# Performance work log

Measured on AMD Instinct MI355X. Metric: run time of the kernel, lower is better.

The kernel has to match this reference:

```python
import jax, jax.numpy as jnp
import numpy as np


def setup_inputs() -> dict:
    key = jax.random.key(0)
    kx, kq, kb, kc = jax.random.split(key, 4)
    N, D = 16384, 1024
    x = jax.random.normal(kx, (N, D), dtype=jnp.float32)
    Q = jax.random.normal(kq, (D, D), dtype=jnp.float32)
    b = jax.random.normal(kb, (D,), dtype=jnp.float32)
    c = jax.random.normal(kc, (1,), dtype=jnp.float32)
    return {"x": x, "Q": Q, "b": b, "c": c}


def reference(x, Q, b, c):
    # y_i = x_i^T Q x_i + b^T x_i + c  (same math as diag(x @ Q @ x.T)
    # without materializing the NxN matrix)
    xQ = x @ Q                                # [N, D]
    quad = jnp.sum(xQ * x, axis=-1)           # [N]
    y = quad + x @ b + c                       # [N] (c broadcasts from [1])
    return y[:, None]                          # [N, 1]
```

## Files before the change

### kernel.cpp

```cpp
#include <hip/hip_runtime.h>
#include <hip/hip_bf16.h>


#define DD 1024
#define KSTEPS 32
#define NTILE 32
#define LDS_ROW 520

typedef short v8s __attribute__((ext_vector_type(8)));
typedef float v4f __attribute__((ext_vector_type(4)));

__device__ __forceinline__ short f2b(float f) {
    union { __hip_bfloat16 h; short s; } u;
    u.h = __float2bfloat16(f);
    return u.s;
}

__global__ __launch_bounds__(512, 2)
void quad_kernel(const float* __restrict__ x, const float* __restrict__ Q,
                 const float* __restrict__ bvec, const float* __restrict__ cptr,
                 float* __restrict__ y)
{
    __shared__ short lq[2][16 * LDS_ROW];

    const int tid  = threadIdx.x;
    const int lane = tid & 63;
    const int wave = tid >> 6;
    const int quad = lane >> 4;
    const int l15  = lane & 15;

    const int half = blockIdx.x >> 7;
    const int rblk = blockIdx.x & 127;
    const int row_base = rblk * 128 + wave * 16;
    const int t0 = half * NTILE;

    const float cc = (half == 0) ? cptr[0] : 0.f;

    v8s afrag[KSTEPS];
    {
        const float* xr = x + (size_t)(row_base + l15) * DD + quad * 8;
        #pragma unroll
        for (int kt = 0; kt < KSTEPS; ++kt) {
            const float4 f0 = *(const float4*)(xr + kt * 32);
            const float4 f1 = *(const float4*)(xr + kt * 32 + 4);
            v8s a;
            a[0]=f2b(f0.x); a[1]=f2b(f0.y); a[2]=f2b(f0.z); a[3]=f2b(f0.w);
            a[4]=f2b(f1.x); a[5]=f2b(f1.y); a[6]=f2b(f1.z); a[7]=f2b(f1.w);
            afrag[kt] = a;
            asm volatile("" : "+a"(afrag[kt]));
        }
    }

    int s_nn[4], s_k4[4];
    #pragma unroll
    for (int i = 0; i < 4; ++i) {
        const int idx = tid + i * 512;
        s_nn[i] = idx >> 7;
        s_k4[i] = idx & 127;
    }

    float4 pf[4];
    #pragma unroll
    for (int i = 0; i < 4; ++i)
        pf[i] = *(const float4*)(Q + (size_t)(t0 * 16 + s_nn[i]) * DD + s_k4[i] * 4);

    float acc[4] = {0.f, 0.f, 0.f, 0.f};
    v4f cf = {0.f, 0.f, 0.f, 0.f};
    float xv[4], bn;

    const short* bp0 = &lq[0][l15 * LDS_ROW + quad * 8];
    const short* bp1 = &lq[1][l15 * LDS_ROW + quad * 8];

    for (int t = 0; t < NTILE; ++t) {
        const int tg = t0 + t;

        #pragma unroll
        for (int i = 0; i < 4; ++i) {
            const float4 f = pf[i];
            short4 s;
            s.x=f2b(f.x); s.y=f2b(f.y); s.z=f2b(f.z); s.w=f2b(f.w);
            *(short4*)&lq[0][s_nn[i] * LDS_ROW + s_k4[i] * 4] = s;
        }
        #pragma unroll
        for (int i = 0; i < 4; ++i)
            pf[i] = *(const float4*)(Q + (size_t)(tg * 16 + s_nn[i]) * DD + 512 + s_k4[i] * 4);
        {
            const int n = tg * 16 + l15;
            bn = bvec[n];
            const float* xc = x + (size_t)(row_base + quad * 4) * DD + n;
            #pragma unroll
            for (int r = 0; r < 4; ++r) xv[r] = xc[(size_t)r * DD];
        }
        __syncthreads();
        #pragma unroll
        for (int s = 0; s < 16; ++s) {
            const v8s bfrag = *(const v8s*)(bp0 + s * 32);
            cf = __builtin_amdgcn_mfma_f32_16x16x32_bf16(afrag[s], bfrag, cf, 0, 0, 0);
        }

        #pragma unroll
        for (int i = 0; i < 4; ++i) {
            const float4 f = pf[i];
            short4 s;
            s.x=f2b(f.x); s.y=f2b(f.y); s.z=f2b(f.z); s.w=f2b(f.w);
            *(short4*)&lq[1][s_nn[i] * LDS_ROW + s_k4[i] * 4] = s;
        }
        if (t + 1 < NTILE) {
            #pragma unroll
            for (int i = 0; i < 4; ++i)
                pf[i] = *(const float4*)(Q + (size_t)((tg + 1) * 16 + s_nn[i]) * DD + s_k4[i] * 4);
        }
        __syncthreads();
        #pragma unroll
        for (int s = 0; s < 16; ++s) {
            const v8s bfrag = *(const v8s*)(bp1 + s * 32);
            cf = __builtin_amdgcn_mfma_f32_16x16x32_bf16(afrag[16 + s], bfrag, cf, 0, 0, 0);
        }

        #pragma unroll
        for (int r = 0; r < 4; ++r) acc[r] += (cf[r] + bn) * xv[r];
        cf = (v4f){0.f, 0.f, 0.f, 0.f};
    }

    #pragma unroll
    for (int r = 0; r < 4; ++r) {
        float v = acc[r];
        v += __shfl_xor(v, 1);
        v += __shfl_xor(v, 2);
        v += __shfl_xor(v, 4);
        v += __shfl_xor(v, 8);
        if (l15 == 0) atomicAdd(&y[row_base + quad * 4 + r], v + cc);
    }
}

extern "C" void kernel_launch(void* const* d_in, const int* in_sizes, int n_in,
                              void* d_out, int out_size, void* d_ws, size_t ws_size,
                              hipStream_t stream)
{
    const float* x = (const float*)d_in[0];
    const float* Q = (const float*)d_in[1];
    const float* b = (const float*)d_in[2];
    const float* c = (const float*)d_in[3];
    float* y = (float*)d_out;

    hipMemsetAsync(y, 0, (size_t)out_size * sizeof(float), stream);
    quad_kernel<<<dim3(256), dim3(512), 0, stream>>>(x, Q, b, c, y);
}
```

Measured before the change: 164.6 us.

## Split work over K-halves and column segments, two row tiles per wave

Each wave now computes two 16-row tiles that share every LDS B-fragment read. The grid is split 8 ways per 256-row block: four column segments times two K halves. Partial quadratic terms are combined with atomics, and the b term is added only on the first K half. Q staging now uses a single sync per tile with alternating LDS buffers. The aim is to halve LDS traffic per MFMA and double the grid. Raising launch bounds to 4 blocks per CU risks register pressure or spills, since each lane holds 32 bf16 A fragments.

```diff
diff --git a/kernel.cpp b/kernel.cpp
--- a/kernel.cpp
+++ b/kernel.cpp
@@ -3,8 +3,9 @@
 
 
 #define DD 1024
-#define KSTEPS 32
-#define NTILE 32
+#define KH 512
+#define KSTEP 16
+#define NT 16
 #define LDS_ROW 520
 
 typedef short v8s __attribute__((ext_vector_type(8)));
@@ -16,7 +17,7 @@
     return u.s;
 }
 
-__global__ __launch_bounds__(512, 2)
+__global__ __launch_bounds__(512, 4)
 void quad_kernel(const float* __restrict__ x, const float* __restrict__ Q,
                  const float* __restrict__ bvec, const float* __restrict__ cptr,
                  float* __restrict__ y)
@@ -29,25 +30,34 @@
     const int quad = lane >> 4;
     const int l15  = lane & 15;
 
-    const int half = blockIdx.x >> 7;
-    const int rblk = blockIdx.x & 127;
-    const int row_base = rblk * 128 + wave * 16;
-    const int t0 = half * NTILE;
+    const int seg    = blockIdx.x & 7;
+    const int rblk   = blockIdx.x >> 3;
+    const int colseg = seg >> 1;
+    const int khalf  = seg & 1;
 
-    const float cc = (half == 0) ? cptr[0] : 0.f;
+    const int row_base = rblk * 256 + wave * 32;
+    const int kofs  = khalf * KH;
+    const int tbase = colseg * NT;
 
-    v8s afrag[KSTEPS];
+    v8s a0[KSTEP], a1[KSTEP];
     {
-        const float* xr = x + (size_t)(row_base + l15) * DD + quad * 8;
+        const float* xr0 = x + (size_t)(row_base + l15) * DD + kofs + quad * 8;
+        const float* xr1 = xr0 + (size_t)16 * DD;
         #pragma unroll
-        for (int kt = 0; kt < KSTEPS; ++kt) {
-            const float4 f0 = *(const float4*)(xr + kt * 32);
-            const float4 f1 = *(const float4*)(xr + kt * 32 + 4);
+        for (int kt = 0; kt < KSTEP; ++kt) {
+            float4 f0 = *(const float4*)(xr0 + kt * 32);
+            float4 f1 = *(const float4*)(xr0 + kt * 32 + 4);
             v8s a;
             a[0]=f2b(f0.x); a[1]=f2b(f0.y); a[2]=f2b(f0.z); a[3]=f2b(f0.w);
             a[4]=f2b(f1.x); a[5]=f2b(f1.y); a[6]=f2b(f1.z); a[7]=f2b(f1.w);
-            afrag[kt] = a;
-            asm volatile("" : "+a"(afrag[kt]));
+            a0[kt] = a;
+            asm volatile("" : "+a"(a0[kt]));
+            f0 = *(const float4*)(xr1 + kt * 32);
+            f1 = *(const float4*)(xr1 + kt * 32 + 4);
+            a[0]=f2b(f0.x); a[1]=f2b(f0.y); a[2]=f2b(f0.z); a[3]=f2b(f0.w);
+            a[4]=f2b(f1.x); a[5]=f2b(f1.y); a[6]=f2b(f1.z); a[7]=f2b(f1.w);
+            a1[kt] = a;
+            asm volatile("" : "+a"(a1[kt]));
         }
     }
 
@@ -62,74 +72,72 @@
     float4 pf[4];
     #pragma unroll
     for (int i = 0; i < 4; ++i)
-        pf[i] = *(const float4*)(Q + (size_t)(t0 * 16 + s_nn[i]) * DD + s_k4[i] * 4);
+        pf[i] = *(const float4*)(Q + (size_t)(tbase * 16 + s_nn[i]) * DD + kofs + s_k4[i] * 4);
 
-    float acc[4] = {0.f, 0.f, 0.f, 0.f};
-    v4f cf = {0.f, 0.f, 0.f, 0.f};
-    float xv[4], bn;
+    float acc0[4] = {0,0,0,0}, acc1[4] = {0,0,0,0};
 
     const short* bp0 = &lq[0][l15 * LDS_ROW + quad * 8];
     const short* bp1 = &lq[1][l15 * LDS_ROW + quad * 8];
 
-    for (int t = 0; t < NTILE; ++t) {
-        const int tg = t0 + t;
+    for (int t = 0; t < NT; ++t) {
+        const int tg = tbase + t;
 
+        short* dst = &lq[t & 1][0];
         #pragma unroll
         for (int i = 0; i < 4; ++i) {
             const float4 f = pf[i];
             short4 s;
             s.x=f2b(f.x); s.y=f2b(f.y); s.z=f2b(f.z); s.w=f2b(f.w);
-            *(short4*)&lq[0][s_nn[i] * LDS_ROW + s_k4[i] * 4] = s;
+            *(short4*)&dst[s_nn[i] * LDS_ROW + s_k4[i] * 4] = s;
         }
-        #pragma unroll
-        for (int i = 0; i < 4; ++i)
-            pf[i] = *(const float4*)(Q + (size_t)(tg * 16 + s_nn[i]) * DD + 512 + s_k4[i] * 4);
+        __syncthreads();
+
+        if (t + 1 < NT) {
+            #pragma unroll
+            for (int i = 0; i < 4; ++i)
+                pf[i] = *(const float4*)(Q + (size_t)((tg + 1) * 16 + s_nn[i]) * DD + kofs + s_k4[i] * 4);
+        }
+
+        const int n = tg * 16 + l15;
+        const float bn = (khalf == 0) ? bvec[n] : 0.f;
+        float xv0[4], xv1[4];
         {
-            const int n = tg * 16 + l15;
-            bn = bvec[n];
             const float* xc = x + (size_t)(row_base + quad * 4) * DD + n;
             #pragma unroll
-            for (int r = 0; r < 4; ++r) xv[r] = xc[(size_t)r * DD];
+            for (int r = 0; r < 4; ++r) {
+                xv0[r] = xc[(size_t)r * DD];
+                xv1[r] = xc[(size_t)(r + 16) * DD];
+            }
         }
-        __syncthreads();
+
+        v4f cf0 = {0,0,0,0}, cf1 = {0,0,0,0};
+        const short* bp = (t & 1) ? bp1 : bp0;
         #pragma unroll
-        for (int s = 0; s < 16; ++s) {
-            const v8s bfrag = *(const v8s*)(bp0 + s * 32);
-            cf = __builtin_amdgcn_mfma_f32_16x16x32_bf16(afrag[s], bfrag, cf, 0, 0, 0);
+        for (int s = 0; s < KSTEP; ++s) {
+            const v8s bfrag = *(const v8s*)(bp + s * 32);
+            cf0 = __builtin_amdgcn_mfma_f32_16x16x32_bf16(a0[s], bfrag, cf0, 0, 0, 0);
+            cf1 = __builtin_amdgcn_mfma_f32_16x16x32_bf16(a1[s], bfrag, cf1, 0, 0, 0);
         }
 
         #pragma unroll
-        for (int i = 0; i < 4; ++i) {
-            const float4 f = pf[i];
-            short4 s;
-            s.x=f2b(f.x); s.y=f2b(f.y); s.z=f2b(f.z); s.w=f2b(f.w);
-            *(short4*)&lq[1][s_nn[i] * LDS_ROW + s_k4[i] * 4] = s;
+        for (int r = 0; r < 4; ++r) {
+            acc0[r] += (cf0[r] + bn) * xv0[r];
+            acc1[r] += (cf1[r] + bn) * xv1[r];
         }
-        if (t + 1 < NTILE) {
-            #pragma unroll
-            for (int i = 0; i < 4; ++i)
-                pf[i] = *(const float4*)(Q + (size_t)((tg + 1) * 16 + s_nn[i]) * DD + s_k4[i] * 4);
-        }
-        __syncthreads();
-        #pragma unroll
-        for (int s = 0; s < 16; ++s) {
-            const v8s bfrag = *(const v8s*)(bp1 + s * 32);
-            cf = __builtin_amdgcn_mfma_f32_16x16x32_bf16(afrag[16 + s], bfrag, cf, 0, 0, 0);
-        }
-
-        #pragma unroll
-        for (int r = 0; r < 4; ++r) acc[r] += (cf[r] + bn) * xv[r];
-        cf = (v4f){0.f, 0.f, 0.f, 0.f};
     }
 
+    const float cc = (seg == 0) ? cptr[0] : 0.f;
     #pragma unroll
     for (int r = 0; r < 4; ++r) {
-        float v = acc[r];
-        v += __shfl_xor(v, 1);
-        v += __shfl_xor(v, 2);
-        v += __shfl_xor(v, 4);
-        v += __shfl_xor(v, 8);
+        float v = acc0[r];
+        v += __shfl_xor(v, 1); v += __shfl_xor(v, 2);
+        v += __shfl_xor(v, 4); v += __shfl_xor(v, 8);
         if (l15 == 0) atomicAdd(&y[row_base + quad * 4 + r], v + cc);
+
+        float w = acc1[r];
+        w += __shfl_xor(w, 1); w += __shfl_xor(w, 2);
+        w += __shfl_xor(w, 4); w += __shfl_xor(w, 8);
+        if (l15 == 0) atomicAdd(&y[row_base + 16 + quad * 4 + r], w + cc);
     }
 }
 
@@ -144,5 +152,5 @@
     float* y = (float*)d_out;
 
     hipMemsetAsync(y, 0, (size_t)out_size * sizeof(float), stream);
-    quad_kernel<<<dim3(256), dim3(512), 0, stream>>>(x, Q, b, c, y);
+    quad_kernel<<<dim3(512), dim3(512), 0, stream>>>(x, Q, b, c, y);
 }
```

New measurement: 332.2 us. 2.02x slower.
